# Performance work log

Measured on AMD Instinct MI355X. Metric: run time of the kernel, lower is better.

The kernel has to match this reference:

```python
import jax, jax.numpy as jnp
import numpy as np
from jax import lax

IMG = 800.0
PRE_NMS = 2000
POST_NMS = 1000
IOU_T = 0.7
BBOX_XFORM_CLIP = float(np.log(1000.0 / 16.0))


def build_anchors():
    # torchvision FPN anchor generator: one size per level, 3 aspect ratios
    strides = [4, 8, 16, 32, 64]
    sizes = [32, 64, 128, 256, 512]
    ratios = [0.5, 1.0, 2.0]
    out = []
    for s, sz in zip(strides, sizes):
        f = int(np.ceil(800 / s))  # feature map side
        base = []
        for r in ratios:
            w = sz * np.sqrt(1.0 / r)
            h = sz * np.sqrt(r)
            base.append([-w / 2, -h / 2, w / 2, h / 2])
        base = np.asarray(base)  # [3,4]
        sx = (np.arange(f) + 0.5) * s
        sy = (np.arange(f) + 0.5) * s
        yy, xx = np.meshgrid(sy, sx, indexing='ij')
        shifts = np.stack([xx, yy, xx, yy], -1).reshape(-1, 1, 4)
        out.append((shifts + base).reshape(-1, 4))
    return np.concatenate(out, 0).astype(np.float32)  # [159882,4]


def setup_inputs() -> dict:
    key = jax.random.key(0)
    k1, k2 = jax.random.split(key)
    B = 16
    anchors = jnp.asarray(build_anchors())
    A = anchors.shape[0]
    scores = jax.random.normal(k1, (B, A), dtype=jnp.float32)
    deltas = jax.random.normal(k2, (B, A, 4), dtype=jnp.float32) * 0.1
    return {"scores": scores, "deltas": deltas, "anchors": anchors}


def decode_boxes(deltas, anchors):
    wa = anchors[:, 2] - anchors[:, 0]
    ha = anchors[:, 3] - anchors[:, 1]
    cxa = anchors[:, 0] + 0.5 * wa
    cya = anchors[:, 1] + 0.5 * ha
    dx, dy = deltas[:, 0], deltas[:, 1]
    dw = jnp.minimum(deltas[:, 2], BBOX_XFORM_CLIP)
    dh = jnp.minimum(deltas[:, 3], BBOX_XFORM_CLIP)
    cx = dx * wa + cxa
    cy = dy * ha + cya
    w = jnp.exp(dw) * wa
    h = jnp.exp(dh) * ha
    boxes = jnp.stack([cx - 0.5 * w, cy - 0.5 * h, cx + 0.5 * w, cy + 0.5 * h], -1)
    return jnp.clip(boxes, 0.0, IMG)


def box_iou(a, b):
    # a: [N,4], b: [M,4]
    area_a = (a[:, 2] - a[:, 0]) * (a[:, 3] - a[:, 1])
    area_b = (b[:, 2] - b[:, 0]) * (b[:, 3] - b[:, 1])
    lt = jnp.maximum(a[:, None, :2], b[None, :, :2])
    rb = jnp.minimum(a[:, None, 2:], b[None, :, 2:])
    wh = jnp.clip(rb - lt, 0.0)
    inter = wh[..., 0] * wh[..., 1]
    return inter / (area_a[:, None] + area_b[None, :] - inter + 1e-9)


def greedy_nms_keep(boxes, iou_t):
    # boxes are sorted by descending score
    K = boxes.shape[0]
    iou = box_iou(boxes, boxes)  # [K,K]
    idx = jnp.arange(K)

    def body(i, keep):
        sup = (iou[i] > iou_t) & keep[i] & (idx > i)
        return keep & ~sup

    return lax.fori_loop(0, K, body, jnp.ones((K,), bool))


def _process_image(scores_i, deltas_i, anchors):
    # top-k pre-NMS on objectness logits (torchvision RPN order)
    top_logits, idx = lax.top_k(scores_i, PRE_NMS)
    boxes = decode_boxes(deltas_i[idx], anchors[idx])  # [PRE,4]
    keep = greedy_nms_keep(boxes, IOU_T)
    masked = jnp.where(keep, top_logits, -jnp.inf)
    kept_logits, idx2 = lax.top_k(masked, POST_NMS)
    kept_boxes = boxes[idx2]
    valid = jnp.isfinite(kept_logits)
    probs = jax.nn.sigmoid(jnp.where(valid, kept_logits, 0.0))
    out_boxes = jnp.where(valid[:, None], kept_boxes, 0.0)
    out_scores = jnp.where(valid, probs, 0.0)
    return jnp.concatenate([out_boxes, out_scores[:, None]], -1)  # [POST,5]


def reference(scores, deltas, anchors):
    return jax.vmap(_process_image, in_axes=(0, 0, None))(scores, deltas, anchors)
```

## Files before the change

### kernel.cpp

```cpp
#include <hip/hip_runtime.h>
#include <math.h>

#define PRE_NMS 2000
#define POST_NMS 1000
#define IOU_T 0.7f
#define IMGSZ 800.0f
#define CAP 6144
#define SORTN 2048
#define NBINS 1024
#define NWORDS 32
#define NSLICE 16
#define MROWS 2048
#define NTILES 528

typedef unsigned long long u64;

__device__ __forceinline__ unsigned key_of(float f) {
    unsigned u = __float_as_uint(f);
    return (u & 0x80000000u) ? ~u : (u | 0x80000000u);
}
__device__ __forceinline__ float inv_key(unsigned k) {
    unsigned u = (k & 0x80000000u) ? (k ^ 0x80000000u) : ~k;
    return __uint_as_float(u);
}

__global__ __launch_bounds__(256) void hist_kernel(
    const float* __restrict__ scores, int A, unsigned* __restrict__ ghist) {
  int b = blockIdx.x, slice = blockIdx.y;
  __shared__ unsigned h[NBINS];
  int tid = threadIdx.x;
  for (int i = tid; i < NBINS; i += 256) h[i] = 0;
  __syncthreads();
  int per = (A + NSLICE - 1) / NSLICE;
  int lo = slice * per, hi = min(lo + per, A);
  const float* sc = scores + (size_t)b * A;
  for (int i = lo + tid; i < hi; i += 256)
    atomicAdd(&h[key_of(sc[i]) >> 22], 1u);
  __syncthreads();
  for (int i = tid; i < NBINS; i += 256)
    if (h[i]) atomicAdd(&ghist[b * NBINS + i], h[i]);
}

__global__ __launch_bounds__(256) void compact_kernel(
    const float* __restrict__ scores, int A, const unsigned* __restrict__ ghist,
    u64* __restrict__ cand, int* __restrict__ cand_cnt, int* __restrict__ T1) {
  int b = blockIdx.x, slice = blockIdx.y;
  int tid = threadIdx.x;
  int lane = tid & 63, wave = tid >> 6;
  __shared__ unsigned sa[2][NBINS];
  __shared__ int sT;
  for (int i = tid; i < NBINS; i += 256) sa[0][i] = ghist[b * NBINS + i];
  __syncthreads();
  int src = 0;
  for (int d = 1; d < NBINS; d <<= 1) {
    for (int i = tid; i < NBINS; i += 256)
      sa[src ^ 1][i] = sa[src][i] + ((i + d < NBINS) ? sa[src][i + d] : 0u);
    __syncthreads();
    src ^= 1;
  }
  for (int i = tid; i < NBINS; i += 256) {
    unsigned v = sa[src][i];
    unsigned nx = (i < NBINS - 1) ? sa[src][i + 1] : 0u;
    if (v >= PRE_NMS && nx < PRE_NMS) sT = i;
  }
  __syncthreads();
  int T = sT;
  if (slice == 0 && tid == 0) T1[b] = T;
  int per = (A + NSLICE - 1) / NSLICE;
  int lo = slice * per, hi = min(lo + per, A);
  const float* sc = scores + (size_t)b * A;
  int cnt = 0;
  for (int i = lo + tid; i < hi; i += 256)
    cnt += ((int)(key_of(sc[i]) >> 22) >= T);
  int pfx = cnt;
  #pragma unroll
  for (int d = 1; d < 64; d <<= 1) {
    int t2 = __shfl_up(pfx, d, 64);
    if (lane >= d) pfx += t2;
  }
  __shared__ int s_wt[4];
  __shared__ int s_base;
  if (lane == 63) s_wt[wave] = pfx;
  __syncthreads();
  if (tid == 0) {
    int tot = s_wt[0] + s_wt[1] + s_wt[2] + s_wt[3];
    int acc = 0;
    #pragma unroll
    for (int w2 = 0; w2 < 4; ++w2) { int t3 = s_wt[w2]; s_wt[w2] = acc; acc += t3; }
    s_base = atomicAdd(&cand_cnt[b], tot);
  }
  __syncthreads();
  int my_off = s_base + s_wt[wave] + (pfx - cnt);
  u64* cb = cand + (size_t)b * CAP;
  for (int i = lo + tid; i < hi; i += 256) {
    unsigned k = key_of(sc[i]);
    if ((int)(k >> 22) >= T) {
      if (my_off < CAP) cb[my_off] = ((u64)k << 32) | (unsigned)(~i);
      my_off++;
    }
  }
}

__global__ __launch_bounds__(1024) void refine_select_kernel(
    const u64* __restrict__ cand, const int* __restrict__ cand_cnt,
    const int* __restrict__ T1,
    u64* __restrict__ gsel, int* __restrict__ sel_cnt) {
  int b = blockIdx.x, tid = threadIdx.x;
  int lane = tid & 63;
  __shared__ unsigned h2[NBINS];
  __shared__ unsigned tmp[NBINS];
  __shared__ int s_above, s_sel, s_T2;
  int n = min(cand_cnt[b], CAP);
  const u64* cb = cand + (size_t)b * CAP;
  h2[tid] = 0;
  if (tid == 0) { s_above = 0; s_sel = 0; }
  __syncthreads();
  int T1v = T1[b];
  int loc = 0;
  for (int i = tid; i < n; i += 1024) {
    unsigned k = (unsigned)(cb[i] >> 32);
    if ((int)(k >> 22) > T1v) loc++;
    else atomicAdd(&h2[(k >> 12) & 1023], 1u);
  }
  for (int d = 32; d; d >>= 1) loc += __shfl_down(loc, d, 64);
  if (lane == 0 && loc) atomicAdd(&s_above, loc);
  __syncthreads();
  unsigned v = h2[tid];
  for (int d = 1; d < NBINS; d <<= 1) {
    tmp[tid] = v;
    __syncthreads();
    if (tid + d < NBINS) v += tmp[tid + d];
    __syncthreads();
  }
  tmp[tid] = v;
  __syncthreads();
  int above = s_above;
  unsigned nextv = (tid < NBINS - 1) ? tmp[tid + 1] : 0u;
  if (above + (int)v >= PRE_NMS && above + (int)nextv < PRE_NMS) s_T2 = tid;
  __syncthreads();
  unsigned thresh20 = ((unsigned)T1v << 10) | (unsigned)s_T2;
  u64* gs = gsel + (size_t)b * SORTN;
  for (int i = tid; i < n; i += 1024) {
    u64 cv = cb[i];
    if ((unsigned)(cv >> 44) >= thresh20) {
      int pos = atomicAdd(&s_sel, 1);
      if (pos < SORTN) gs[pos] = cv;
    }
  }
  __syncthreads();
  if (tid == 0) sel_cnt[b] = min(s_sel, SORTN);
}

__global__ __launch_bounds__(256) void rank_decode_kernel(
    const u64* __restrict__ gsel, const int* __restrict__ sel_cnt,
    const float* __restrict__ deltas, const float* __restrict__ anchors, int A,
    float* __restrict__ boxes, float* __restrict__ topk_logit) {
  int b = blockIdx.x, ci = blockIdx.y;
  int tid = threadIdx.x;
  __shared__ u64 keys[SORTN];
  __shared__ int s_part[256];
  const u64* gs = gsel + (size_t)b * SORTN;
  int n = sel_cnt[b];
  for (int i = tid; i < SORTN; i += 256)
    keys[i] = (i < n) ? gs[i] : 0ULL;
  __syncthreads();
  int half = tid >> 7;
  int li = tid & 127;
  int i = ci * 128 + li;
  u64 my = keys[i];
  int rank = 0;
  const ulonglong2* k2 = (const ulonglong2*)(keys + half * (SORTN / 2));
  #pragma unroll 4
  for (int j = 0; j < SORTN / 4; ++j) {
    ulonglong2 kk = k2[j];
    rank += (kk.x > my) + (kk.y > my);
  }
  s_part[tid] = rank;
  __syncthreads();
  if (half == 0) {
    rank = s_part[tid] + s_part[tid + 128];
    if (i < n && rank < PRE_NMS) {
      int a = (int)(~(unsigned)my);
      topk_logit[b * PRE_NMS + rank] = inv_key((unsigned)(my >> 32));
      const float CLIP = 4.135166556742356f;
      float4 dl = ((const float4*)deltas)[(size_t)b * A + a];
      float4 an = ((const float4*)anchors)[a];
      float wa = __fsub_rn(an.z, an.x);
      float ha = __fsub_rn(an.w, an.y);
      float cxa = __fadd_rn(an.x, __fmul_rn(0.5f, wa));
      float cya = __fadd_rn(an.y, __fmul_rn(0.5f, ha));
      float dw = fminf(dl.z, CLIP), dh = fminf(dl.w, CLIP);
      float cx = __fadd_rn(__fmul_rn(dl.x, wa), cxa);
      float cy = __fadd_rn(__fmul_rn(dl.y, ha), cya);
      float w2 = __fmul_rn((float)exp((double)dw), wa);
      float h2f = __fmul_rn((float)exp((double)dh), ha);
      float x1 = __fsub_rn(cx, __fmul_rn(0.5f, w2));
      float y1 = __fsub_rn(cy, __fmul_rn(0.5f, h2f));
      float x2 = __fadd_rn(cx, __fmul_rn(0.5f, w2));
      float y2 = __fadd_rn(cy, __fmul_rn(0.5f, h2f));
      x1 = fminf(fmaxf(x1, 0.f), IMGSZ);
      y1 = fminf(fmaxf(y1, 0.f), IMGSZ);
      x2 = fminf(fmaxf(x2, 0.f), IMGSZ);
      y2 = fminf(fmaxf(y2, 0.f), IMGSZ);
      ((float4*)boxes)[(size_t)b * PRE_NMS + rank] = make_float4(x1, y1, x2, y2);
    }
  }
}

__global__ __launch_bounds__(64) void iou_tile(
    const float* __restrict__ boxes, u64* __restrict__ maskT,
    unsigned* __restrict__ tflag) {
  int k = blockIdx.x;
  int b = blockIdx.y;
  int wj = (int)((sqrtf(8.0f * k + 1.0f) - 1.0f) * 0.5f);
  while ((wj + 1) * (wj + 2) / 2 <= k) ++wj;
  while (wj * (wj + 1) / 2 > k) --wj;
  int ti = k - wj * (wj + 1) / 2;
  int lane = threadIdx.x;
  int i = ti * 64 + lane;
  const float4* bb = (const float4*)boxes + (size_t)b * PRE_NMS;
  __shared__ float4 sbox[64];
  int jg = wj * 64 + lane;
  sbox[lane] = bb[min(jg, PRE_NMS - 1)];
  float4 A4 = bb[min(i, PRE_NMS - 1)];
  __syncthreads();
  float area_a = __fmul_rn(__fsub_rn(A4.z, A4.x), __fsub_rn(A4.w, A4.y));
  u64 m = 0;
  #pragma unroll 8
  for (int jj = 0; jj < 64; ++jj) {
    float4 Bb = sbox[jj];
    float area_b = __fmul_rn(__fsub_rn(Bb.z, Bb.x), __fsub_rn(Bb.w, Bb.y));
    float ltx = fmaxf(A4.x, Bb.x), lty = fmaxf(A4.y, Bb.y);
    float rbx = fminf(A4.z, Bb.z), rby = fminf(A4.w, Bb.w);
    float iw = fmaxf(__fsub_rn(rbx, ltx), 0.f);
    float ih = fmaxf(__fsub_rn(rby, lty), 0.f);
    float inter = __fmul_rn(iw, ih);
    float denom = __fadd_rn(__fsub_rn(__fadd_rn(area_a, area_b), inter), 1e-9f);
    float iou = inter / denom;
    int j = wj * 64 + jj;
    if (j > i && iou > IOU_T) m |= 1ULL << jj;
  }
  maskT[((size_t)b * NWORDS + wj) * MROWS + i] = m;
  u64 anyb = __ballot(m != 0ULL);
  if (lane == 0) tflag[(size_t)b * NTILES + k] = (anyb != 0ULL) ? 1u : 0u;
}

#define WSTRIDE 65
#define BAR_LDS() asm volatile("s_waitcnt lgkmcnt(0)\n\ts_barrier" ::: "memory")
__global__ __launch_bounds__(256, 1) void nms_scan(
    const u64* __restrict__ maskT, const unsigned* __restrict__ tflag,
    const float* __restrict__ boxes,
    const float* __restrict__ logits, float* __restrict__ out) {
  int b = blockIdx.x;
  int tid = threadIdx.x;
  int wave = tid >> 6, lane = tid & 63;
  __shared__ u64 buf[3][NWORDS * WSTRIDE];
  __shared__ u64 s_keep[NWORDS];
  __shared__ u64 s_cur[2];
  __shared__ unsigned char sflag[NTILES];
  const unsigned* tf = tflag + (size_t)b * NTILES;
  for (int i2 = tid; i2 < NTILES; i2 += 256)
    sflag[i2] = (unsigned char)(tf[i2] != 0u);
  if (tid < NWORDS) s_keep[tid] = (tid == NWORDS - 1) ? 0xFFFFULL : ~0ULL;
  const u64* mb = maskT + (size_t)b * NWORDS * MROWS;
  int w = tid >> 3;
  int sub = tid & 7;
  uint4 nx0, nx1, nx2, nx3;
  {
    const uint4* src = (const uint4*)(mb + (size_t)w * MROWS + sub * 8);
    uint4 a0 = src[0], a1 = src[1], a2 = src[2], a3 = src[3];
    u64* dst = &buf[0][w * WSTRIDE + sub * 8];
    dst[0] = ((u64)a0.y << 32) | a0.x;  dst[1] = ((u64)a0.w << 32) | a0.z;
    dst[2] = ((u64)a1.y << 32) | a1.x;  dst[3] = ((u64)a1.w << 32) | a1.z;
    dst[4] = ((u64)a2.y << 32) | a2.x;  dst[5] = ((u64)a2.w << 32) | a2.z;
    dst[6] = ((u64)a3.y << 32) | a3.x;  dst[7] = ((u64)a3.w << 32) | a3.z;
  }
  bool have = (w >= 1);
  if (have) {
    const uint4* src = (const uint4*)(mb + (size_t)w * MROWS + 64 + sub * 8);
    nx0 = src[0]; nx1 = src[1]; nx2 = src[2]; nx3 = src[3];
  }
  BAR_LDS();
  for (int c = 0; c < NWORDS; ++c) {
    if (c + 1 < NWORDS && have) {
      u64* dst = &buf[(c + 1) % 3][w * WSTRIDE + sub * 8];
      dst[0] = ((u64)nx0.y << 32) | nx0.x;  dst[1] = ((u64)nx0.w << 32) | nx0.z;
      dst[2] = ((u64)nx1.y << 32) | nx1.x;  dst[3] = ((u64)nx1.w << 32) | nx1.z;
      dst[4] = ((u64)nx2.y << 32) | nx2.x;  dst[5] = ((u64)nx2.w << 32) | nx2.z;
      dst[6] = ((u64)nx3.y << 32) | nx3.x;  dst[7] = ((u64)nx3.w << 32) | nx3.z;
    }
    have = false;
    if (c + 2 < NWORDS && w >= c + 2 &&
        sflag[(w * (w + 1)) / 2 + (c + 2)]) {
      const uint4* src = (const uint4*)(mb + (size_t)w * MROWS + (c + 2) * 64 + sub * 8);
      nx0 = src[0]; nx1 = src[1]; nx2 = src[2]; nx3 = src[3];
      have = true;
    }
    if (wave == 0) {
      u64 k0 = s_keep[c];
      u64 cur;
      if (sflag[(c * (c + 3)) >> 1]) {
        u64 diag = buf[c % 3][c * WSTRIDE + lane];
        unsigned dlo = (unsigned)diag, dhi = (unsigned)(diag >> 32);
        unsigned clo = __builtin_amdgcn_readfirstlane((unsigned)k0);
        unsigned chi = __builtin_amdgcn_readfirstlane((unsigned)(k0 >> 32));
        #pragma unroll
        for (int bb = 0; bb < 32; ++bb) {
          unsigned rlo = __builtin_amdgcn_readlane(dlo, bb);
          unsigned rhi = __builtin_amdgcn_readlane(dhi, bb);
          unsigned msk = 0u - ((clo >> bb) & 1u);
          clo &= ~(rlo & msk);
          chi &= ~(rhi & msk);
        }
        #pragma unroll
        for (int bb = 0; bb < 32; ++bb) {
          unsigned rlo = __builtin_amdgcn_readlane(dlo, bb + 32);
          unsigned rhi = __builtin_amdgcn_readlane(dhi, bb + 32);
          unsigned msk = 0u - ((chi >> bb) & 1u);
          clo &= ~(rlo & msk);
          chi &= ~(rhi & msk);
        }
        cur = ((u64)chi << 32) | clo;
      } else {
        cur = k0;
      }
      if (lane == 0) { s_keep[c] = cur; s_cur[c & 1] = cur; }
      if (c + 1 < NWORDS && sflag[(((c + 1) * (c + 2)) >> 1) + c]) {
        u64 row = buf[c % 3][(c + 1) * WSTRIDE + lane];
        u64 bit = (cur >> lane) & 1ULL;
        u64 v = row & (0ULL - bit);
        v |= __shfl_xor(v, 1, 64);
        v |= __shfl_xor(v, 2, 64);
        v |= __shfl_xor(v, 4, 64);
        v |= __shfl_xor(v, 8, 64);
        v |= __shfl_xor(v, 16, 64);
        v |= __shfl_xor(v, 32, 64);
        if (lane == 0 && v) atomicAnd(&s_keep[c + 1], ~v);
      }
    } else if (c >= 1) {
      u64 kept = s_cur[(c - 1) & 1];
      int g = lane >> 3, s = lane & 7;
      const u64* bbuf = &buf[(c - 1) % 3][0];
      for (int idx = (wave - 1) + 3 * g; idx < NWORDS - 1 - c; idx += 24) {
        int w2 = c + 1 + idx;
        if (!sflag[(w2 * (w2 + 1)) / 2 + (c - 1)]) continue;
        u64 v = 0;
        #pragma unroll
        for (int k = 0; k < 8; ++k) {
          int r = s + 8 * k;
          u64 bit = (kept >> r) & 1ULL;
          v |= bbuf[w2 * WSTRIDE + r] & (0ULL - bit);
        }
        v |= __shfl_xor(v, 1, 64);
        v |= __shfl_xor(v, 2, 64);
        v |= __shfl_xor(v, 4, 64);
        if (s == 0 && v) atomicAnd(&s_keep[w2], ~v);
      }
    }
    BAR_LDS();
  }
  __shared__ int pre[NWORDS];
  __shared__ int s_tot;
  if (tid == 0) {
    int acc = 0;
    for (int ww = 0; ww < NWORDS; ++ww) {
      pre[ww] = acc;
      acc += __popcll(s_keep[ww]);
    }
    s_tot = acc;
  }
  __syncthreads();
  const float* lg_b = logits + b * PRE_NMS;
  const float4* bx_b = (const float4*)boxes + (size_t)b * PRE_NMS;
  for (int i = tid; i < PRE_NMS; i += 256) {
    u64 wv = s_keep[i >> 6];
    if ((wv >> (i & 63)) & 1) {
      int rank = pre[i >> 6] + __popcll(wv & ((1ULL << (i & 63)) - 1ULL));
      if (rank < POST_NMS) {
        float4 bx = bx_b[i];
        float lg = lg_b[i];
        float e = (float)exp(-(double)lg);
        float pp = 1.0f / (1.0f + e);
        float* o = out + ((size_t)b * POST_NMS + rank) * 5;
        o[0] = bx.x; o[1] = bx.y; o[2] = bx.z; o[3] = bx.w; o[4] = pp;
      }
    }
  }
  int tot = s_tot;
  for (int j = tid; j < POST_NMS; j += 256) {
    if (j >= tot) {
      float* o = out + ((size_t)b * POST_NMS + j) * 5;
      o[0] = 0.f; o[1] = 0.f; o[2] = 0.f; o[3] = 0.f; o[4] = 0.f;
    }
  }
}

extern "C" void kernel_launch(void* const* d_in, const int* in_sizes, int n_in,
                              void* d_out, int out_size, void* d_ws, size_t ws_size,
                              hipStream_t stream) {
  const float* scores  = (const float*)d_in[0];
  const float* deltas  = (const float*)d_in[1];
  const float* anchors = (const float*)d_in[2];
  int A = in_sizes[2] / 4;
  int B = in_sizes[0] / A;

  char* ws = (char*)d_ws;
  size_t off = 0;
  auto alloc = [&](size_t bytes) {
    void* p = ws + off;
    off += (bytes + 255) & ~(size_t)255;
    return p;
  };
  unsigned* ghist    = (unsigned*)alloc((size_t)B * NBINS * 4);
  int*      cand_cnt = (int*)alloc((size_t)B * 4);
  size_t zero_bytes = off;
  int*      T1       = (int*)alloc((size_t)B * 4);
  u64*      cand     = (u64*)alloc((size_t)B * CAP * 8);
  u64*      gsel     = (u64*)alloc((size_t)B * SORTN * 8);
  int*      sel_cnt  = (int*)alloc((size_t)B * 4);
  float*    topk_lg  = (float*)alloc((size_t)B * PRE_NMS * 4);
  float*    boxes    = (float*)alloc((size_t)B * PRE_NMS * 16);
  u64*      maskT    = (u64*)alloc((size_t)B * NWORDS * MROWS * 8);
  unsigned* tflag    = (unsigned*)alloc((size_t)B * NTILES * 4);

  hipMemsetAsync(ws, 0, zero_bytes, stream);

  hist_kernel<<<dim3(B, NSLICE), 256, 0, stream>>>(scores, A, ghist);
  compact_kernel<<<dim3(B, NSLICE), 256, 0, stream>>>(scores, A, ghist, cand, cand_cnt, T1);
  refine_select_kernel<<<B, 1024, 0, stream>>>(cand, cand_cnt, T1, gsel, sel_cnt);
  rank_decode_kernel<<<dim3(B, SORTN / 128), 256, 0, stream>>>(
      gsel, sel_cnt, deltas, anchors, A, boxes, topk_lg);
  int ntiles = NTILES;
  iou_tile<<<dim3(ntiles, B), 64, 0, stream>>>(boxes, maskT, tflag);
  nms_scan<<<B, 256, 0, stream>>>(maskT, tflag, boxes, topk_lg, (float*)d_out);
}
```

Measured before the change: 204.3 us.

## Fuse NMS pipeline into one cooperative kernel with grid syncs

Replaces the memset and six separate kernel launches with a single cooperative kernel of B*16 blocks that runs each stage in turn, separated by grid.sync(). Each slice now writes its own histogram, summed afterwards, instead of atomically adding into a zeroed global one. This removes the memset and per-launch overhead and gaps. In exchange, some stages run on only B blocks while the rest idle at the grid barrier, and refine runs with 256 threads instead of 1024.

New measurement: 385.4 us. 1.89x slower.

```diff
diff --git a/kernel.cpp b/kernel.cpp
--- a/kernel.cpp
+++ b/kernel.cpp
@@ -1,5 +1,8 @@
 #include <hip/hip_runtime.h>
+#include <hip/hip_cooperative_groups.h>
 #include <math.h>
+
+namespace cg = cooperative_groups;
 
 #define PRE_NMS 2000
 #define POST_NMS 1000
@@ -12,6 +15,7 @@
 #define NSLICE 16
 #define MROWS 2048
 #define NTILES 528
+#define WSTRIDE 65
 
 typedef unsigned long long u64;
 
@@ -24,373 +28,387 @@
     return __uint_as_float(u);
 }
 
-__global__ __launch_bounds__(256) void hist_kernel(
-    const float* __restrict__ scores, int A, unsigned* __restrict__ ghist) {
-  int b = blockIdx.x, slice = blockIdx.y;
-  __shared__ unsigned h[NBINS];
-  int tid = threadIdx.x;
-  for (int i = tid; i < NBINS; i += 256) h[i] = 0;
-  __syncthreads();
-  int per = (A + NSLICE - 1) / NSLICE;
-  int lo = slice * per, hi = min(lo + per, A);
-  const float* sc = scores + (size_t)b * A;
-  for (int i = lo + tid; i < hi; i += 256)
-    atomicAdd(&h[key_of(sc[i]) >> 22], 1u);
-  __syncthreads();
-  for (int i = tid; i < NBINS; i += 256)
-    if (h[i]) atomicAdd(&ghist[b * NBINS + i], h[i]);
-}
-
-__global__ __launch_bounds__(256) void compact_kernel(
-    const float* __restrict__ scores, int A, const unsigned* __restrict__ ghist,
-    u64* __restrict__ cand, int* __restrict__ cand_cnt, int* __restrict__ T1) {
-  int b = blockIdx.x, slice = blockIdx.y;
+#define BAR_LDS() asm volatile("s_waitcnt lgkmcnt(0)\n\ts_barrier" ::: "memory")
+
+union SMem {
+  struct { unsigned h[NBINS]; } p1;
+  struct { unsigned sa[2][NBINS]; int sT; int s_wt[4]; int s_base; } p2;
+  struct { unsigned h2[NBINS]; unsigned tmp[NBINS];
+           int s_above, s_sel, s_T2; } p3;
+  struct { u64 keys[SORTN]; int s_part[256]; } p4;
+  struct { float4 sbox[4][64]; } p5;
+  struct { u64 buf[3][NWORDS * WSTRIDE]; u64 s_keep[NWORDS]; u64 s_cur[2];
+           unsigned char sflag[NTILES]; int pre[NWORDS]; int s_tot; } p6;
+};
+
+__global__ __launch_bounds__(256, 1) void fused_pipeline(
+    const float* __restrict__ scores, const float* __restrict__ deltas,
+    const float* __restrict__ anchors, int A, int B,
+    unsigned* __restrict__ ghist, int* __restrict__ T1,
+    u64* __restrict__ cand, int* __restrict__ cand_cnt,
+    u64* __restrict__ gsel, int* __restrict__ sel_cnt,
+    float* __restrict__ topk_logit, float* __restrict__ boxes,
+    u64* __restrict__ maskT, unsigned* __restrict__ tflag,
+    float* __restrict__ out) {
+  cg::grid_group grid = cg::this_grid();
+  __shared__ SMem sm;
+  int bid = blockIdx.x;
   int tid = threadIdx.x;
   int lane = tid & 63, wave = tid >> 6;
-  __shared__ unsigned sa[2][NBINS];
-  __shared__ int sT;
-  for (int i = tid; i < NBINS; i += 256) sa[0][i] = ghist[b * NBINS + i];
-  __syncthreads();
-  int src = 0;
-  for (int d = 1; d < NBINS; d <<= 1) {
-    for (int i = tid; i < NBINS; i += 256)
-      sa[src ^ 1][i] = sa[src][i] + ((i + d < NBINS) ? sa[src][i + d] : 0u);
-    __syncthreads();
-    src ^= 1;
-  }
-  for (int i = tid; i < NBINS; i += 256) {
-    unsigned v = sa[src][i];
-    unsigned nx = (i < NBINS - 1) ? sa[src][i + 1] : 0u;
-    if (v >= PRE_NMS && nx < PRE_NMS) sT = i;
-  }
-  __syncthreads();
-  int T = sT;
-  if (slice == 0 && tid == 0) T1[b] = T;
-  int per = (A + NSLICE - 1) / NSLICE;
-  int lo = slice * per, hi = min(lo + per, A);
-  const float* sc = scores + (size_t)b * A;
-  int cnt = 0;
-  for (int i = lo + tid; i < hi; i += 256)
-    cnt += ((int)(key_of(sc[i]) >> 22) >= T);
-  int pfx = cnt;
-  #pragma unroll
-  for (int d = 1; d < 64; d <<= 1) {
-    int t2 = __shfl_up(pfx, d, 64);
-    if (lane >= d) pfx += t2;
-  }
-  __shared__ int s_wt[4];
-  __shared__ int s_base;
-  if (lane == 63) s_wt[wave] = pfx;
-  __syncthreads();
-  if (tid == 0) {
-    int tot = s_wt[0] + s_wt[1] + s_wt[2] + s_wt[3];
-    int acc = 0;
+
+  {
+    int b = bid >> 4, slice = bid & 15;
+    unsigned* h = sm.p1.h;
+    for (int i = tid; i < NBINS; i += 256) h[i] = 0;
+    if (slice == 0 && tid == 0) cand_cnt[b] = 0;
+    __syncthreads();
+    int per = (A + NSLICE - 1) / NSLICE;
+    int lo = slice * per, hi = min(lo + per, A);
+    const float* sc = scores + (size_t)b * A;
+    for (int i = lo + tid; i < hi; i += 256)
+      atomicAdd(&h[key_of(sc[i]) >> 22], 1u);
+    __syncthreads();
+    unsigned* gh = ghist + ((size_t)b * NSLICE + slice) * NBINS;
+    for (int i = tid; i < NBINS; i += 256) gh[i] = h[i];
+  }
+  grid.sync();
+
+  {
+    int b = bid >> 4, slice = bid & 15;
+    for (int i = tid; i < NBINS; i += 256) {
+      unsigned s = 0;
+      const unsigned* gh = ghist + (size_t)b * NSLICE * NBINS + i;
+      #pragma unroll
+      for (int s16 = 0; s16 < NSLICE; ++s16) s += gh[s16 * NBINS];
+      sm.p2.sa[0][i] = s;
+    }
+    __syncthreads();
+    int src = 0;
+    for (int d = 1; d < NBINS; d <<= 1) {
+      for (int i = tid; i < NBINS; i += 256)
+        sm.p2.sa[src ^ 1][i] = sm.p2.sa[src][i] +
+            ((i + d < NBINS) ? sm.p2.sa[src][i + d] : 0u);
+      __syncthreads();
+      src ^= 1;
+    }
+    for (int i = tid; i < NBINS; i += 256) {
+      unsigned v = sm.p2.sa[src][i];
+      unsigned nx = (i < NBINS - 1) ? sm.p2.sa[src][i + 1] : 0u;
+      if (v >= PRE_NMS && nx < PRE_NMS) sm.p2.sT = i;
+    }
+    __syncthreads();
+    int T = sm.p2.sT;
+    if (slice == 0 && tid == 0) T1[b] = T;
+    int per = (A + NSLICE - 1) / NSLICE;
+    int lo = slice * per, hi = min(lo + per, A);
+    const float* sc = scores + (size_t)b * A;
+    int cnt = 0;
+    for (int i = lo + tid; i < hi; i += 256)
+      cnt += ((int)(key_of(sc[i]) >> 22) >= T);
+    int pfx = cnt;
     #pragma unroll
-    for (int w2 = 0; w2 < 4; ++w2) { int t3 = s_wt[w2]; s_wt[w2] = acc; acc += t3; }
-    s_base = atomicAdd(&cand_cnt[b], tot);
-  }
-  __syncthreads();
-  int my_off = s_base + s_wt[wave] + (pfx - cnt);
-  u64* cb = cand + (size_t)b * CAP;
-  for (int i = lo + tid; i < hi; i += 256) {
-    unsigned k = key_of(sc[i]);
-    if ((int)(k >> 22) >= T) {
-      if (my_off < CAP) cb[my_off] = ((u64)k << 32) | (unsigned)(~i);
-      my_off++;
-    }
-  }
-}
-
-__global__ __launch_bounds__(1024) void refine_select_kernel(
-    const u64* __restrict__ cand, const int* __restrict__ cand_cnt,
-    const int* __restrict__ T1,
-    u64* __restrict__ gsel, int* __restrict__ sel_cnt) {
-  int b = blockIdx.x, tid = threadIdx.x;
-  int lane = tid & 63;
-  __shared__ unsigned h2[NBINS];
-  __shared__ unsigned tmp[NBINS];
-  __shared__ int s_above, s_sel, s_T2;
-  int n = min(cand_cnt[b], CAP);
-  const u64* cb = cand + (size_t)b * CAP;
-  h2[tid] = 0;
-  if (tid == 0) { s_above = 0; s_sel = 0; }
-  __syncthreads();
-  int T1v = T1[b];
-  int loc = 0;
-  for (int i = tid; i < n; i += 1024) {
-    unsigned k = (unsigned)(cb[i] >> 32);
-    if ((int)(k >> 22) > T1v) loc++;
-    else atomicAdd(&h2[(k >> 12) & 1023], 1u);
-  }
-  for (int d = 32; d; d >>= 1) loc += __shfl_down(loc, d, 64);
-  if (lane == 0 && loc) atomicAdd(&s_above, loc);
-  __syncthreads();
-  unsigned v = h2[tid];
-  for (int d = 1; d < NBINS; d <<= 1) {
-    tmp[tid] = v;
-    __syncthreads();
-    if (tid + d < NBINS) v += tmp[tid + d];
-    __syncthreads();
-  }
-  tmp[tid] = v;
-  __syncthreads();
-  int above = s_above;
-  unsigned nextv = (tid < NBINS - 1) ? tmp[tid + 1] : 0u;
-  if (above + (int)v >= PRE_NMS && above + (int)nextv < PRE_NMS) s_T2 = tid;
-  __syncthreads();
-  unsigned thresh20 = ((unsigned)T1v << 10) | (unsigned)s_T2;
-  u64* gs = gsel + (size_t)b * SORTN;
-  for (int i = tid; i < n; i += 1024) {
-    u64 cv = cb[i];
-    if ((unsigned)(cv >> 44) >= thresh20) {
-      int pos = atomicAdd(&s_sel, 1);
-      if (pos < SORTN) gs[pos] = cv;
-    }
-  }
-  __syncthreads();
-  if (tid == 0) sel_cnt[b] = min(s_sel, SORTN);
-}
-
-__global__ __launch_bounds__(256) void rank_decode_kernel(
-    const u64* __restrict__ gsel, const int* __restrict__ sel_cnt,
-    const float* __restrict__ deltas, const float* __restrict__ anchors, int A,
-    float* __restrict__ boxes, float* __restrict__ topk_logit) {
-  int b = blockIdx.x, ci = blockIdx.y;
-  int tid = threadIdx.x;
-  __shared__ u64 keys[SORTN];
-  __shared__ int s_part[256];
-  const u64* gs = gsel + (size_t)b * SORTN;
-  int n = sel_cnt[b];
-  for (int i = tid; i < SORTN; i += 256)
-    keys[i] = (i < n) ? gs[i] : 0ULL;
-  __syncthreads();
-  int half = tid >> 7;
-  int li = tid & 127;
-  int i = ci * 128 + li;
-  u64 my = keys[i];
-  int rank = 0;
-  const ulonglong2* k2 = (const ulonglong2*)(keys + half * (SORTN / 2));
-  #pragma unroll 4
-  for (int j = 0; j < SORTN / 4; ++j) {
-    ulonglong2 kk = k2[j];
-    rank += (kk.x > my) + (kk.y > my);
-  }
-  s_part[tid] = rank;
-  __syncthreads();
-  if (half == 0) {
-    rank = s_part[tid] + s_part[tid + 128];
-    if (i < n && rank < PRE_NMS) {
-      int a = (int)(~(unsigned)my);
-      topk_logit[b * PRE_NMS + rank] = inv_key((unsigned)(my >> 32));
-      const float CLIP = 4.135166556742356f;
-      float4 dl = ((const float4*)deltas)[(size_t)b * A + a];
-      float4 an = ((const float4*)anchors)[a];
-      float wa = __fsub_rn(an.z, an.x);
-      float ha = __fsub_rn(an.w, an.y);
-      float cxa = __fadd_rn(an.x, __fmul_rn(0.5f, wa));
-      float cya = __fadd_rn(an.y, __fmul_rn(0.5f, ha));
-      float dw = fminf(dl.z, CLIP), dh = fminf(dl.w, CLIP);
-      float cx = __fadd_rn(__fmul_rn(dl.x, wa), cxa);
-      float cy = __fadd_rn(__fmul_rn(dl.y, ha), cya);
-      float w2 = __fmul_rn((float)exp((double)dw), wa);
-      float h2f = __fmul_rn((float)exp((double)dh), ha);
-      float x1 = __fsub_rn(cx, __fmul_rn(0.5f, w2));
-      float y1 = __fsub_rn(cy, __fmul_rn(0.5f, h2f));
-      float x2 = __fadd_rn(cx, __fmul_rn(0.5f, w2));
-      float y2 = __fadd_rn(cy, __fmul_rn(0.5f, h2f));
-      x1 = fminf(fmaxf(x1, 0.f), IMGSZ);
-      y1 = fminf(fmaxf(y1, 0.f), IMGSZ);
-      x2 = fminf(fmaxf(x2, 0.f), IMGSZ);
-      y2 = fminf(fmaxf(y2, 0.f), IMGSZ);
-      ((float4*)boxes)[(size_t)b * PRE_NMS + rank] = make_float4(x1, y1, x2, y2);
-    }
-  }
-}
-
-__global__ __launch_bounds__(64) void iou_tile(
-    const float* __restrict__ boxes, u64* __restrict__ maskT,
-    unsigned* __restrict__ tflag) {
-  int k = blockIdx.x;
-  int b = blockIdx.y;
-  int wj = (int)((sqrtf(8.0f * k + 1.0f) - 1.0f) * 0.5f);
-  while ((wj + 1) * (wj + 2) / 2 <= k) ++wj;
-  while (wj * (wj + 1) / 2 > k) --wj;
-  int ti = k - wj * (wj + 1) / 2;
-  int lane = threadIdx.x;
-  int i = ti * 64 + lane;
-  const float4* bb = (const float4*)boxes + (size_t)b * PRE_NMS;
-  __shared__ float4 sbox[64];
-  int jg = wj * 64 + lane;
-  sbox[lane] = bb[min(jg, PRE_NMS - 1)];
-  float4 A4 = bb[min(i, PRE_NMS - 1)];
-  __syncthreads();
-  float area_a = __fmul_rn(__fsub_rn(A4.z, A4.x), __fsub_rn(A4.w, A4.y));
-  u64 m = 0;
-  #pragma unroll 8
-  for (int jj = 0; jj < 64; ++jj) {
-    float4 Bb = sbox[jj];
-    float area_b = __fmul_rn(__fsub_rn(Bb.z, Bb.x), __fsub_rn(Bb.w, Bb.y));
-    float ltx = fmaxf(A4.x, Bb.x), lty = fmaxf(A4.y, Bb.y);
-    float rbx = fminf(A4.z, Bb.z), rby = fminf(A4.w, Bb.w);
-    float iw = fmaxf(__fsub_rn(rbx, ltx), 0.f);
-    float ih = fmaxf(__fsub_rn(rby, lty), 0.f);
-    float inter = __fmul_rn(iw, ih);
-    float denom = __fadd_rn(__fsub_rn(__fadd_rn(area_a, area_b), inter), 1e-9f);
-    float iou = inter / denom;
-    int j = wj * 64 + jj;
-    if (j > i && iou > IOU_T) m |= 1ULL << jj;
-  }
-  maskT[((size_t)b * NWORDS + wj) * MROWS + i] = m;
-  u64 anyb = __ballot(m != 0ULL);
-  if (lane == 0) tflag[(size_t)b * NTILES + k] = (anyb != 0ULL) ? 1u : 0u;
-}
-
-#define WSTRIDE 65
-#define BAR_LDS() asm volatile("s_waitcnt lgkmcnt(0)\n\ts_barrier" ::: "memory")
-__global__ __launch_bounds__(256, 1) void nms_scan(
-    const u64* __restrict__ maskT, const unsigned* __restrict__ tflag,
-    const float* __restrict__ boxes,
-    const float* __restrict__ logits, float* __restrict__ out) {
-  int b = blockIdx.x;
-  int tid = threadIdx.x;
-  int wave = tid >> 6, lane = tid & 63;
-  __shared__ u64 buf[3][NWORDS * WSTRIDE];
-  __shared__ u64 s_keep[NWORDS];
-  __shared__ u64 s_cur[2];
-  __shared__ unsigned char sflag[NTILES];
-  const unsigned* tf = tflag + (size_t)b * NTILES;
-  for (int i2 = tid; i2 < NTILES; i2 += 256)
-    sflag[i2] = (unsigned char)(tf[i2] != 0u);
-  if (tid < NWORDS) s_keep[tid] = (tid == NWORDS - 1) ? 0xFFFFULL : ~0ULL;
-  const u64* mb = maskT + (size_t)b * NWORDS * MROWS;
-  int w = tid >> 3;
-  int sub = tid & 7;
-  uint4 nx0, nx1, nx2, nx3;
+    for (int d = 1; d < 64; d <<= 1) {
+      int t2 = __shfl_up(pfx, d, 64);
+      if (lane >= d) pfx += t2;
+    }
+    if (lane == 63) sm.p2.s_wt[wave] = pfx;
+    __syncthreads();
+    if (tid == 0) {
+      int tot = sm.p2.s_wt[0] + sm.p2.s_wt[1] + sm.p2.s_wt[2] + sm.p2.s_wt[3];
+      int acc = 0;
+      #pragma unroll
+      for (int w2 = 0; w2 < 4; ++w2) {
+        int t3 = sm.p2.s_wt[w2]; sm.p2.s_wt[w2] = acc; acc += t3;
+      }
+      sm.p2.s_base = atomicAdd(&cand_cnt[b], tot);
+    }
+    __syncthreads();
+    int my_off = sm.p2.s_base + sm.p2.s_wt[wave] + (pfx - cnt);
+    u64* cb = cand + (size_t)b * CAP;
+    for (int i = lo + tid; i < hi; i += 256) {
+      unsigned k = key_of(sc[i]);
+      if ((int)(k >> 22) >= T) {
+        if (my_off < CAP) cb[my_off] = ((u64)k << 32) | (unsigned)(~i);
+        my_off++;
+      }
+    }
+  }
+  grid.sync();
+
+  if (bid < B) {
+    int b = bid;
+    unsigned* h2 = sm.p3.h2;
+    unsigned* tp = sm.p3.tmp;
+    int n = min(cand_cnt[b], CAP);
+    const u64* cb = cand + (size_t)b * CAP;
+    for (int i = tid; i < NBINS; i += 256) h2[i] = 0;
+    if (tid == 0) { sm.p3.s_above = 0; sm.p3.s_sel = 0; }
+    __syncthreads();
+    int T1v = T1[b];
+    int loc = 0;
+    for (int i = tid; i < n; i += 256) {
+      unsigned k = (unsigned)(cb[i] >> 32);
+      if ((int)(k >> 22) > T1v) loc++;
+      else atomicAdd(&h2[(k >> 12) & 1023], 1u);
+    }
+    for (int d = 32; d; d >>= 1) loc += __shfl_down(loc, d, 64);
+    if (lane == 0 && loc) atomicAdd(&sm.p3.s_above, loc);
+    __syncthreads();
+    unsigned* bufs[2] = {h2, tp};
+    int src = 0;
+    for (int d = 1; d < NBINS; d <<= 1) {
+      for (int i = tid; i < NBINS; i += 256)
+        bufs[src ^ 1][i] = bufs[src][i] +
+            ((i + d < NBINS) ? bufs[src][i + d] : 0u);
+      __syncthreads();
+      src ^= 1;
+    }
+    int above = sm.p3.s_above;
+    for (int i = tid; i < NBINS; i += 256) {
+      unsigned v = bufs[src][i];
+      unsigned nx = (i < NBINS - 1) ? bufs[src][i + 1] : 0u;
+      if (above + (int)v >= PRE_NMS && above + (int)nx < PRE_NMS)
+        sm.p3.s_T2 = i;
+    }
+    __syncthreads();
+    unsigned thresh20 = ((unsigned)T1v << 10) | (unsigned)sm.p3.s_T2;
+    u64* gs = gsel + (size_t)b * SORTN;
+    for (int i = tid; i < n; i += 256) {
+      u64 cv = cb[i];
+      if ((unsigned)(cv >> 44) >= thresh20) {
+        int pos = atomicAdd(&sm.p3.s_sel, 1);
+        if (pos < SORTN) gs[pos] = cv;
+      }
+    }
+    __syncthreads();
+    if (tid == 0) sel_cnt[b] = min(sm.p3.s_sel, SORTN);
+  }
+  grid.sync();
+
   {
-    const uint4* src = (const uint4*)(mb + (size_t)w * MROWS + sub * 8);
-    uint4 a0 = src[0], a1 = src[1], a2 = src[2], a3 = src[3];
-    u64* dst = &buf[0][w * WSTRIDE + sub * 8];
-    dst[0] = ((u64)a0.y << 32) | a0.x;  dst[1] = ((u64)a0.w << 32) | a0.z;
-    dst[2] = ((u64)a1.y << 32) | a1.x;  dst[3] = ((u64)a1.w << 32) | a1.z;
-    dst[4] = ((u64)a2.y << 32) | a2.x;  dst[5] = ((u64)a2.w << 32) | a2.z;
-    dst[6] = ((u64)a3.y << 32) | a3.x;  dst[7] = ((u64)a3.w << 32) | a3.z;
-  }
-  bool have = (w >= 1);
-  if (have) {
-    const uint4* src = (const uint4*)(mb + (size_t)w * MROWS + 64 + sub * 8);
-    nx0 = src[0]; nx1 = src[1]; nx2 = src[2]; nx3 = src[3];
-  }
-  BAR_LDS();
-  for (int c = 0; c < NWORDS; ++c) {
-    if (c + 1 < NWORDS && have) {
-      u64* dst = &buf[(c + 1) % 3][w * WSTRIDE + sub * 8];
-      dst[0] = ((u64)nx0.y << 32) | nx0.x;  dst[1] = ((u64)nx0.w << 32) | nx0.z;
-      dst[2] = ((u64)nx1.y << 32) | nx1.x;  dst[3] = ((u64)nx1.w << 32) | nx1.z;
-      dst[4] = ((u64)nx2.y << 32) | nx2.x;  dst[5] = ((u64)nx2.w << 32) | nx2.z;
-      dst[6] = ((u64)nx3.y << 32) | nx3.x;  dst[7] = ((u64)nx3.w << 32) | nx3.z;
-    }
-    have = false;
-    if (c + 2 < NWORDS && w >= c + 2 &&
-        sflag[(w * (w + 1)) / 2 + (c + 2)]) {
-      const uint4* src = (const uint4*)(mb + (size_t)w * MROWS + (c + 2) * 64 + sub * 8);
+    int b = bid >> 4, ci = bid & 15;
+    const u64* gs = gsel + (size_t)b * SORTN;
+    int n = sel_cnt[b];
+    for (int i = tid; i < SORTN; i += 256)
+      sm.p4.keys[i] = (i < n) ? gs[i] : 0ULL;
+    __syncthreads();
+    int half = tid >> 7;
+    int li = tid & 127;
+    int i = ci * 128 + li;
+    u64 my = sm.p4.keys[i];
+    int rank = 0;
+    const ulonglong2* k2 = (const ulonglong2*)(sm.p4.keys + half * (SORTN / 2));
+    #pragma unroll 4
+    for (int j = 0; j < SORTN / 4; ++j) {
+      ulonglong2 kk = k2[j];
+      rank += (kk.x > my) + (kk.y > my);
+    }
+    sm.p4.s_part[tid] = rank;
+    __syncthreads();
+    if (half == 0) {
+      rank = sm.p4.s_part[tid] + sm.p4.s_part[tid + 128];
+      if (i < n && rank < PRE_NMS) {
+        int a = (int)(~(unsigned)my);
+        topk_logit[b * PRE_NMS + rank] = inv_key((unsigned)(my >> 32));
+        const float CLIP = 4.135166556742356f;
+        float4 dl = ((const float4*)deltas)[(size_t)b * A + a];
+        float4 an = ((const float4*)anchors)[a];
+        float wa = __fsub_rn(an.z, an.x);
+        float ha = __fsub_rn(an.w, an.y);
+        float cxa = __fadd_rn(an.x, __fmul_rn(0.5f, wa));
+        float cya = __fadd_rn(an.y, __fmul_rn(0.5f, ha));
+        float dw = fminf(dl.z, CLIP), dh = fminf(dl.w, CLIP);
+        float cx = __fadd_rn(__fmul_rn(dl.x, wa), cxa);
+        float cy = __fadd_rn(__fmul_rn(dl.y, ha), cya);
+        float w2 = __fmul_rn((float)exp((double)dw), wa);
+        float h2f = __fmul_rn((float)exp((double)dh), ha);
+        float x1 = __fsub_rn(cx, __fmul_rn(0.5f, w2));
+        float y1 = __fsub_rn(cy, __fmul_rn(0.5f, h2f));
+        float x2 = __fadd_rn(cx, __fmul_rn(0.5f, w2));
+        float y2 = __fadd_rn(cy, __fmul_rn(0.5f, h2f));
+        x1 = fminf(fmaxf(x1, 0.f), IMGSZ);
+        y1 = fminf(fmaxf(y1, 0.f), IMGSZ);
+        x2 = fminf(fmaxf(x2, 0.f), IMGSZ);
+        y2 = fminf(fmaxf(y2, 0.f), IMGSZ);
+        ((float4*)boxes)[(size_t)b * PRE_NMS + rank] = make_float4(x1, y1, x2, y2);
+      }
+    }
+  }
+  grid.sync();
+
+  {
+    int nwaves = gridDim.x * 4;
+    int gw = bid * 4 + wave;
+    float4* sbx = sm.p5.sbox[wave];
+    for (int t = gw; t < NTILES * B; t += nwaves) {
+      int b = t / NTILES;
+      int k = t - b * NTILES;
+      int wj = (int)((sqrtf(8.0f * k + 1.0f) - 1.0f) * 0.5f);
+      while ((wj + 1) * (wj + 2) / 2 <= k) ++wj;
+      while (wj * (wj + 1) / 2 > k) --wj;
+      int ti = k - wj * (wj + 1) / 2;
+      int i = ti * 64 + lane;
+      const float4* bb = (const float4*)boxes + (size_t)b * PRE_NMS;
+      int jg = wj * 64 + lane;
+      sbx[lane] = bb[min(jg, PRE_NMS - 1)];
+      float4 A4 = bb[min(i, PRE_NMS - 1)];
+      float area_a = __fmul_rn(__fsub_rn(A4.z, A4.x), __fsub_rn(A4.w, A4.y));
+      u64 m = 0;
+      #pragma unroll 8
+      for (int jj = 0; jj < 64; ++jj) {
+        float4 Bb = sbx[jj];
+        float area_b = __fmul_rn(__fsub_rn(Bb.z, Bb.x), __fsub_rn(Bb.w, Bb.y));
+        float ltx = fmaxf(A4.x, Bb.x), lty = fmaxf(A4.y, Bb.y);
+        float rbx = fminf(A4.z, Bb.z), rby = fminf(A4.w, Bb.w);
+        float iw = fmaxf(__fsub_rn(rbx, ltx), 0.f);
+        float ih = fmaxf(__fsub_rn(rby, lty), 0.f);
+        float inter = __fmul_rn(iw, ih);
+        float denom = __fadd_rn(__fsub_rn(__fadd_rn(area_a, area_b), inter), 1e-9f);
+        float iou = inter / denom;
+        int j = wj * 64 + jj;
+        if (j > i && iou > IOU_T) m |= 1ULL << jj;
+      }
+      maskT[((size_t)b * NWORDS + wj) * MROWS + i] = m;
+      u64 anyb = __ballot(m != 0ULL);
+      if (lane == 0) tflag[(size_t)b * NTILES + k] = (anyb != 0ULL) ? 1u : 0u;
+    }
+  }
+  grid.sync();
+
+  if (bid < B) {
+    int b = bid;
+    const unsigned* tf = tflag + (size_t)b * NTILES;
+    for (int i2 = tid; i2 < NTILES; i2 += 256)
+      sm.p6.sflag[i2] = (unsigned char)(tf[i2] != 0u);
+    if (tid < NWORDS) sm.p6.s_keep[tid] = (tid == NWORDS - 1) ? 0xFFFFULL : ~0ULL;
+    const u64* mb = maskT + (size_t)b * NWORDS * MROWS;
+    int w = tid >> 3;
+    int sub = tid & 7;
+    uint4 nx0, nx1, nx2, nx3;
+    {
+      const uint4* src = (const uint4*)(mb + (size_t)w * MROWS + sub * 8);
+      uint4 a0 = src[0], a1 = src[1], a2 = src[2], a3 = src[3];
+      u64* dst = &sm.p6.buf[0][w * WSTRIDE + sub * 8];
+      dst[0] = ((u64)a0.y << 32) | a0.x;  dst[1] = ((u64)a0.w << 32) | a0.z;
+      dst[2] = ((u64)a1.y << 32) | a1.x;  dst[3] = ((u64)a1.w << 32) | a1.z;
+      dst[4] = ((u64)a2.y << 32) | a2.x;  dst[5] = ((u64)a2.w << 32) | a2.z;
+      dst[6] = ((u64)a3.y << 32) | a3.x;  dst[7] = ((u64)a3.w << 32) | a3.z;
+    }
+    bool have = (w >= 1);
+    if (have) {
+      const uint4* src = (const uint4*)(mb + (size_t)w * MROWS + 64 + sub * 8);
       nx0 = src[0]; nx1 = src[1]; nx2 = src[2]; nx3 = src[3];
-      have = true;
-    }
-    if (wave == 0) {
-      u64 k0 = s_keep[c];
-      u64 cur;
-      if (sflag[(c * (c + 3)) >> 1]) {
-        u64 diag = buf[c % 3][c * WSTRIDE + lane];
-        unsigned dlo = (unsigned)diag, dhi = (unsigned)(diag >> 32);
-        unsigned clo = __builtin_amdgcn_readfirstlane((unsigned)k0);
-        unsigned chi = __builtin_amdgcn_readfirstlane((unsigned)(k0 >> 32));
-        #pragma unroll
-        for (int bb = 0; bb < 32; ++bb) {
-          unsigned rlo = __builtin_amdgcn_readlane(dlo, bb);
-          unsigned rhi = __builtin_amdgcn_readlane(dhi, bb);
-          unsigned msk = 0u - ((clo >> bb) & 1u);
-          clo &= ~(rlo & msk);
-          chi &= ~(rhi & msk);
+    }
+    BAR_LDS();
+    for (int c = 0; c < NWORDS; ++c) {
+      if (c + 1 < NWORDS && have) {
+        u64* dst = &sm.p6.buf[(c + 1) % 3][w * WSTRIDE + sub * 8];
+        dst[0] = ((u64)nx0.y << 32) | nx0.x;  dst[1] = ((u64)nx0.w << 32) | nx0.z;
+        dst[2] = ((u64)nx1.y << 32) | nx1.x;  dst[3] = ((u64)nx1.w << 32) | nx1.z;
+        dst[4] = ((u64)nx2.y << 32) | nx2.x;  dst[5] = ((u64)nx2.w << 32) | nx2.z;
+        dst[6] = ((u64)nx3.y << 32) | nx3.x;  dst[7] = ((u64)nx3.w << 32) | nx3.z;
+      }
+      have = false;
+      if (c + 2 < NWORDS && w >= c + 2 &&
+          sm.p6.sflag[(w * (w + 1)) / 2 + (c + 2)]) {
+        const uint4* src = (const uint4*)(mb + (size_t)w * MROWS + (c + 2) * 64 + sub * 8);
+        nx0 = src[0]; nx1 = src[1]; nx2 = src[2]; nx3 = src[3];
+        have = true;
+      }
+      if (wave == 0) {
+        u64 k0 = sm.p6.s_keep[c];
+        u64 cur;
+        if (sm.p6.sflag[(c * (c + 3)) >> 1]) {
+          u64 diag = sm.p6.buf[c % 3][c * WSTRIDE + lane];
+          unsigned dlo = (unsigned)diag, dhi = (unsigned)(diag >> 32);
+          unsigned clo = __builtin_amdgcn_readfirstlane((unsigned)k0);
+          unsigned chi = __builtin_amdgcn_readfirstlane((unsigned)(k0 >> 32));
+          #pragma unroll
+          for (int bb = 0; bb < 32; ++bb) {
+            unsigned rlo = __builtin_amdgcn_readlane(dlo, bb);
+            unsigned rhi = __builtin_amdgcn_readlane(dhi, bb);
+            unsigned msk = 0u - ((clo >> bb) & 1u);
+            clo &= ~(rlo & msk);
+            chi &= ~(rhi & msk);
+          }
+          #pragma unroll
+          for (int bb = 0; bb < 32; ++bb) {
+            unsigned rlo = __builtin_amdgcn_readlane(dlo, bb + 32);
+            unsigned rhi = __builtin_amdgcn_readlane(dhi, bb + 32);
+            unsigned msk = 0u - ((chi >> bb) & 1u);
+            clo &= ~(rlo & msk);
+            chi &= ~(rhi & msk);
+          }
+          cur = ((u64)chi << 32) | clo;
+        } else {
+          cur = k0;
         }
-        #pragma unroll
-        for (int bb = 0; bb < 32; ++bb) {
-          unsigned rlo = __builtin_amdgcn_readlane(dlo, bb + 32);
-          unsigned rhi = __builtin_amdgcn_readlane(dhi, bb + 32);
-          unsigned msk = 0u - ((chi >> bb) & 1u);
-          clo &= ~(rlo & msk);
-          chi &= ~(rhi & msk);
+        if (lane == 0) { sm.p6.s_keep[c] = cur; sm.p6.s_cur[c & 1] = cur; }
+        if (c + 1 < NWORDS && sm.p6.sflag[(((c + 1) * (c + 2)) >> 1) + c]) {
+          u64 row = sm.p6.buf[c % 3][(c + 1) * WSTRIDE + lane];
+          u64 bit = (cur >> lane) & 1ULL;
+          u64 v = row & (0ULL - bit);
+          v |= __shfl_xor(v, 1, 64);
+          v |= __shfl_xor(v, 2, 64);
+          v |= __shfl_xor(v, 4, 64);
+          v |= __shfl_xor(v, 8, 64);
+          v |= __shfl_xor(v, 16, 64);
+          v |= __shfl_xor(v, 32, 64);
+          if (lane == 0 && v) atomicAnd(&sm.p6.s_keep[c + 1], ~v);
         }
-        cur = ((u64)chi << 32) | clo;
-      } else {
-        cur = k0;
-      }
-      if (lane == 0) { s_keep[c] = cur; s_cur[c & 1] = cur; }
-      if (c + 1 < NWORDS && sflag[(((c + 1) * (c + 2)) >> 1) + c]) {
-        u64 row = buf[c % 3][(c + 1) * WSTRIDE + lane];
-        u64 bit = (cur >> lane) & 1ULL;
-        u64 v = row & (0ULL - bit);
-        v |= __shfl_xor(v, 1, 64);
-        v |= __shfl_xor(v, 2, 64);
-        v |= __shfl_xor(v, 4, 64);
-        v |= __shfl_xor(v, 8, 64);
-        v |= __shfl_xor(v, 16, 64);
-        v |= __shfl_xor(v, 32, 64);
-        if (lane == 0 && v) atomicAnd(&s_keep[c + 1], ~v);
-      }
-    } else if (c >= 1) {
-      u64 kept = s_cur[(c - 1) & 1];
-      int g = lane >> 3, s = lane & 7;
-      const u64* bbuf = &buf[(c - 1) % 3][0];
-      for (int idx = (wave - 1) + 3 * g; idx < NWORDS - 1 - c; idx += 24) {
-        int w2 = c + 1 + idx;
-        if (!sflag[(w2 * (w2 + 1)) / 2 + (c - 1)]) continue;
-        u64 v = 0;
-        #pragma unroll
-        for (int k = 0; k < 8; ++k) {
-          int r = s + 8 * k;
-          u64 bit = (kept >> r) & 1ULL;
-          v |= bbuf[w2 * WSTRIDE + r] & (0ULL - bit);
+      } else if (c >= 1) {
+        u64 kept = sm.p6.s_cur[(c - 1) & 1];
+        int g = lane >> 3, s = lane & 7;
+        const u64* bbuf = &sm.p6.buf[(c - 1) % 3][0];
+        for (int idx = (wave - 1) + 3 * g; idx < NWORDS - 1 - c; idx += 24) {
+          int w2 = c + 1 + idx;
+          if (!sm.p6.sflag[(w2 * (w2 + 1)) / 2 + (c - 1)]) continue;
+          u64 v = 0;
+          #pragma unroll
+          for (int k = 0; k < 8; ++k) {
+            int r = s + 8 * k;
+            u64 bit = (kept >> r) & 1ULL;
+            v |= bbuf[w2 * WSTRIDE + r] & (0ULL - bit);
+          }
+          v |= __shfl_xor(v, 1, 64);
+          v |= __shfl_xor(v, 2, 64);
+          v |= __shfl_xor(v, 4, 64);
+          if (s == 0 && v) atomicAnd(&sm.p6.s_keep[w2], ~v);
         }
-        v |= __shfl_xor(v, 1, 64);
-        v |= __shfl_xor(v, 2, 64);
-        v |= __shfl_xor(v, 4, 64);
-        if (s == 0 && v) atomicAnd(&s_keep[w2], ~v);
-      }
-    }
-    BAR_LDS();
-  }
-  __shared__ int pre[NWORDS];
-  __shared__ int s_tot;
-  if (tid == 0) {
-    int acc = 0;
-    for (int ww = 0; ww < NWORDS; ++ww) {
-      pre[ww] = acc;
-      acc += __popcll(s_keep[ww]);
-    }
-    s_tot = acc;
-  }
-  __syncthreads();
-  const float* lg_b = logits + b * PRE_NMS;
-  const float4* bx_b = (const float4*)boxes + (size_t)b * PRE_NMS;
-  for (int i = tid; i < PRE_NMS; i += 256) {
-    u64 wv = s_keep[i >> 6];
-    if ((wv >> (i & 63)) & 1) {
-      int rank = pre[i >> 6] + __popcll(wv & ((1ULL << (i & 63)) - 1ULL));
-      if (rank < POST_NMS) {
-        float4 bx = bx_b[i];
-        float lg = lg_b[i];
-        float e = (float)exp(-(double)lg);
-        float pp = 1.0f / (1.0f + e);
-        float* o = out + ((size_t)b * POST_NMS + rank) * 5;
-        o[0] = bx.x; o[1] = bx.y; o[2] = bx.z; o[3] = bx.w; o[4] = pp;
-      }
-    }
-  }
-  int tot = s_tot;
-  for (int j = tid; j < POST_NMS; j += 256) {
-    if (j >= tot) {
-      float* o = out + ((size_t)b * POST_NMS + j) * 5;
-      o[0] = 0.f; o[1] = 0.f; o[2] = 0.f; o[3] = 0.f; o[4] = 0.f;
+      }
+      BAR_LDS();
+    }
+    if (tid == 0) {
+      int acc = 0;
+      for (int ww = 0; ww < NWORDS; ++ww) {
+        sm.p6.pre[ww] = acc;
+        acc += __popcll(sm.p6.s_keep[ww]);
+      }
+      sm.p6.s_tot = acc;
+    }
+    __syncthreads();
+    const float* lg_b = topk_logit + b * PRE_NMS;
+    const float4* bx_b = (const float4*)boxes + (size_t)b * PRE_NMS;
+    for (int i = tid; i < PRE_NMS; i += 256) {
+      u64 wv = sm.p6.s_keep[i >> 6];
+      if ((wv >> (i & 63)) & 1) {
+        int rank = sm.p6.pre[i >> 6] + __popcll(wv & ((1ULL << (i & 63)) - 1ULL));
+        if (rank < POST_NMS) {
+          float4 bx = bx_b[i];
+          float lg = lg_b[i];
+          float e = (float)exp(-(double)lg);
+          float pp = 1.0f / (1.0f + e);
+          float* o = out + ((size_t)b * POST_NMS + rank) * 5;
+          o[0] = bx.x; o[1] = bx.y; o[2] = bx.z; o[3] = bx.w; o[4] = pp;
+        }
+      }
+    }
+    int tot = sm.p6.s_tot;
+    for (int j = tid; j < POST_NMS; j += 256) {
+      if (j >= tot) {
+        float* o = out + ((size_t)b * POST_NMS + j) * 5;
+        o[0] = 0.f; o[1] = 0.f; o[2] = 0.f; o[3] = 0.f; o[4] = 0.f;
+      }
     }
   }
 }
@@ -411,9 +429,8 @@
     off += (bytes + 255) & ~(size_t)255;
     return p;
   };
-  unsigned* ghist    = (unsigned*)alloc((size_t)B * NBINS * 4);
+  unsigned* ghist    = (unsigned*)alloc((size_t)B * NSLICE * NBINS * 4);
   int*      cand_cnt = (int*)alloc((size_t)B * 4);
-  size_t zero_bytes = off;
   int*      T1       = (int*)alloc((size_t)B * 4);
   u64*      cand     = (u64*)alloc((size_t)B * CAP * 8);
   u64*      gsel     = (u64*)alloc((size_t)B * SORTN * 8);
@@ -423,14 +440,13 @@
   u64*      maskT    = (u64*)alloc((size_t)B * NWORDS * MROWS * 8);
   unsigned* tflag    = (unsigned*)alloc((size_t)B * NTILES * 4);
 
-  hipMemsetAsync(ws, 0, zero_bytes, stream);
-
-  hist_kernel<<<dim3(B, NSLICE), 256, 0, stream>>>(scores, A, ghist);
-  compact_kernel<<<dim3(B, NSLICE), 256, 0, stream>>>(scores, A, ghist, cand, cand_cnt, T1);
-  refine_select_kernel<<<B, 1024, 0, stream>>>(cand, cand_cnt, T1, gsel, sel_cnt);
-  rank_decode_kernel<<<dim3(B, SORTN / 128), 256, 0, stream>>>(
-      gsel, sel_cnt, deltas, anchors, A, boxes, topk_lg);
-  int ntiles = NTILES;
-  iou_tile<<<dim3(ntiles, B), 64, 0, stream>>>(boxes, maskT, tflag);
-  nms_scan<<<B, 256, 0, stream>>>(maskT, tflag, boxes, topk_lg, (float*)d_out);
+  float* out_f = (float*)d_out;
+  void* args[] = {
+    (void*)&scores, (void*)&deltas, (void*)&anchors, (void*)&A, (void*)&B,
+    (void*)&ghist, (void*)&T1, (void*)&cand, (void*)&cand_cnt,
+    (void*)&gsel, (void*)&sel_cnt, (void*)&topk_lg, (void*)&boxes,
+    (void*)&maskT, (void*)&tflag, (void*)&out_f
+  };
+  hipLaunchCooperativeKernel(reinterpret_cast<const void*>(fused_pipeline),
+                             dim3(B * NSLICE), dim3(256), args, 0, stream);
 }
```
